# Performance work log

Measured on AMD Instinct MI355X. Metric: run time of the kernel, lower is better.

The kernel has to match this reference:

```python
import jax, jax.numpy as jnp
import numpy as np

SEQ_LEN = 2048
N_FFT = 4096  # nearest power of two >= 2*SEQ_LEN - 1
K = 24
D_IN = 512
D_OUT = 512
K_U = 3


def setup_inputs() -> dict:
    key = jax.random.key(0)
    k1, k2, k3, k4, k5 = jax.random.split(key, 5)
    x = jax.random.normal(k1, (1, SEQ_LEN, D_IN), dtype=jnp.float32)
    phi = jax.random.normal(k2, (SEQ_LEN, K), dtype=jnp.float32)
    M = jax.random.normal(k3, (D_OUT, D_IN, K_U), dtype=jnp.float32) / D_IN
    M_phi_plus = jax.random.normal(k4, (K, D_IN, D_OUT), dtype=jnp.float32) / 10.0
    M_phi_minus = jax.random.normal(k5, (K, D_IN, D_OUT), dtype=jnp.float32) / 10.0
    return {"x": x, "phi": phi, "M": M, "M_phi_plus": M_phi_plus, "M_phi_minus": M_phi_minus}


def _convolve(u, v, n):
    # u: (bsz, seq, d_in); v: (seq, K) spectral filters
    bsz, seq_len, d_in = u.shape
    Kf = v.shape[1]
    # alternating sign (+1, -1, +1, ...) along time, shape (1, seq, 1, 1)
    sgn = jnp.where(jnp.arange(seq_len) % 2 == 1, -1.0, 1.0).reshape(1, seq_len, 1, 1)
    v_f = jnp.fft.rfft(v.astype(jnp.float32).reshape(1, seq_len, Kf, 1, 1), n=n, axis=1)
    u_exp = jnp.broadcast_to(u[:, :, None, :], (bsz, seq_len, Kf, d_in))
    # stack [u, u*sgn] -> (bsz, seq, K, d_in, 2)
    U = jnp.stack([u_exp, u_exp * sgn], axis=-1).astype(jnp.float32)
    U_f = jnp.fft.rfft(U, n=n, axis=1)
    U_conv = jnp.fft.irfft(v_f * U_f, n=n, axis=1)[:, :seq_len]
    U_plus = U_conv[..., 0]
    U_minus = U_conv[..., 1] * sgn  # (b, seq, K, d_in) * (1, seq, 1, 1)
    return U_plus, U_minus


def _ar_preds(M, x):
    # M: (d_out, d_in, k_u); x: (b, l, d_in)
    # ar[t] = sum_{i=0}^{k_u-1} M[:,:,i] @ x[t-i]  (zero before start)
    b, l, _ = x.shape
    out = jnp.zeros((b, l, M.shape[0]), dtype=x.dtype)
    for i in range(M.shape[-1]):
        x_shift = jnp.pad(x, ((0, 0), (i, 0), (0, 0)))[:, :l]
        out = out + jnp.einsum("bli,oi->blo", x_shift, M[:, :, i])
    return out


def reference(x, phi, M, M_phi_plus, M_phi_minus):
    U_plus, U_minus = _convolve(x, phi, N_FFT)
    spectral_plus = jnp.einsum("blkd,kdo->blo", U_plus, M_phi_plus)
    spectral_minus = jnp.einsum("blkd,kdo->blo", U_minus, M_phi_minus)
    output = spectral_plus + spectral_minus  # use_hankel_L=False
    ar = _ar_preds(M, x)
    return output + ar
```

## Files before the change

kernel.cpp:

```cpp
#include <hip/hip_runtime.h>

typedef __bf16 bf16;
typedef bf16 bf16x8 __attribute__((ext_vector_type(8)));
typedef float floatx16 __attribute__((ext_vector_type(16)));

#define AS1 __attribute__((address_space(1)))
#define AS3 __attribute__((address_space(3)))

#define KTOT 26112

__device__ __forceinline__ void stage_tile(const bf16* g, int ld, bf16* lds, int tid) {
#pragma unroll
    for (int it = 0; it < 4; ++it) {
        int q    = it * 256 + tid;
        int row  = q >> 3;
        int col8 = (q & 7) ^ (row & 7);
        __builtin_amdgcn_global_load_lds(
            (const AS1 void*)(g + (size_t)row * ld + col8 * 8),
            (AS3 void*)(lds + q * 8), 16, 0, 0);
    }
}

__device__ __forceinline__ void mfma_block(const bf16* lA, const bf16* lB,
                                           floatx16 acc[2][2], int lane, int wm, int wn) {
    const int lrow = lane & 31;
    const int lk   = lane >> 5;
#pragma unroll
    for (int s = 0; s < 4; ++s) {
        bf16x8 af[2], bfr[2];
        const int c8 = s * 2 + lk;
#pragma unroll
        for (int mi = 0; mi < 2; ++mi) {
            int r = wm * 64 + mi * 32 + lrow;
            af[mi] = *(const bf16x8*)(lA + r * 64 + ((c8 ^ (r & 7)) << 3));
        }
#pragma unroll
        for (int ni = 0; ni < 2; ++ni) {
            int r = wn * 64 + ni * 32 + lrow;
            bfr[ni] = *(const bf16x8*)(lB + r * 64 + ((c8 ^ (r & 7)) << 3));
        }
#pragma unroll
        for (int mi = 0; mi < 2; ++mi)
#pragma unroll
            for (int ni = 0; ni < 2; ++ni)
                acc[mi][ni] = __builtin_amdgcn_mfma_f32_32x32x16_bf16(
                    af[mi], bfr[ni], acc[mi][ni], 0, 0, 0);
    }
}

#define CD_ROW(r, lane) (((r) & 3) + 8 * ((r) >> 2) + 4 * ((lane) >> 5))

__global__ __launch_bounds__(256) void conv_gemm(const bf16* __restrict__ Tb,
                                                 const bf16* __restrict__ xT2,
                                                 bf16* __restrict__ A2) {
    __shared__ bf16 lA[128 * 64], lB[128 * 64];
    const int tid = threadIdx.x;
    const int lane = tid & 63, wave = tid >> 6, wm = wave & 1, wn = wave >> 1;
    const int bid = blockIdx.x;
    const int a    = 7 - (bid / 384);
    const int rem  = bid % 384;
    const int dblk = rem / 48;
    const int kw   = rem % 48;

    floatx16 acc[2][2];
#pragma unroll
    for (int mi = 0; mi < 2; ++mi)
#pragma unroll
        for (int ni = 0; ni < 2; ++ni)
#pragma unroll
            for (int e = 0; e < 16; ++e) acc[mi][ni][e] = 0.f;

    for (int c = 0; c <= a; ++c) {
        const bf16* Ab = Tb + ((size_t)kw * 8 + (a - c)) * 16384;
        const bf16* Bb = xT2 + (size_t)(dblk * 128) * 1024 + c * 128;
#pragma unroll
        for (int kk = 0; kk < 128; kk += 64) {
            stage_tile(Ab + kk, 128, lA, tid);
            stage_tile(Bb + kk, 1024, lB, tid);
            __syncthreads();
            mfma_block(lA, lB, acc, lane, wm, wn);
            __syncthreads();
        }
    }
    const int w = kw & 1, k = kw >> 1;
    const int kv = w ? (24 + k) : k;
    const int p = dblk >> 2, dbase = (dblk & 3) * 128;
    bf16* Ocol = A2 + (size_t)kv * 512 + dbase;
#pragma unroll
    for (int mi = 0; mi < 2; ++mi)
#pragma unroll
        for (int ni = 0; ni < 2; ++ni)
#pragma unroll
            for (int r = 0; r < 16; ++r) {
                int tau = a * 128 + wm * 64 + mi * 32 + CD_ROW(r, lane);
                int t = 2 * tau + p + w;
                if (t < 2048) {
                    int col = wn * 64 + ni * 32 + (lane & 31);
                    Ocol[(size_t)t * KTOT + col] = (bf16)acc[mi][ni][r];
                }
            }
}

__global__ __launch_bounds__(256) void proj_gemm(const bf16* __restrict__ A2,
                                                 const bf16* __restrict__ B2,
                                                 float* __restrict__ P2) {
    __shared__ bf16 lA[128 * 64], lB[128 * 64];
    const int tid = threadIdx.x;
    const int lane = tid & 63, wave = tid >> 6, wm = wave & 1, wn = wave >> 1;
    const int bm = blockIdx.x, sp = blockIdx.y, bn = blockIdx.z;
    const bf16* Ab = A2 + (size_t)bm * 128 * KTOT + sp * 2176;
    const bf16* Bb = B2 + (size_t)bn * 128 * KTOT + sp * 2176;

    floatx16 acc[2][2];
#pragma unroll
    for (int mi = 0; mi < 2; ++mi)
#pragma unroll
        for (int ni = 0; ni < 2; ++ni)
#pragma unroll
            for (int e = 0; e < 16; ++e) acc[mi][ni][e] = 0.f;

    for (int kk = 0; kk < 2176; kk += 64) {
        stage_tile(Ab + kk, KTOT, lA, tid);
        stage_tile(Bb + kk, KTOT, lB, tid);
        __syncthreads();
        mfma_block(lA, lB, acc, lane, wm, wn);
        __syncthreads();
    }
    float* Pt = P2 + (size_t)sp * 1048576;
#pragma unroll
    for (int mi = 0; mi < 2; ++mi)
#pragma unroll
        for (int ni = 0; ni < 2; ++ni)
#pragma unroll
            for (int r = 0; r < 16; ++r) {
                int t = bm * 128 + wm * 64 + mi * 32 + CD_ROW(r, lane);
                int o = bn * 128 + wn * 64 + ni * 32 + (lane & 31);
                Pt[(size_t)t * 512 + o] = acc[mi][ni][r];
            }
}

__global__ void prep_all(const float* __restrict__ x, const float* __restrict__ phi,
                         const float* __restrict__ M, const float* __restrict__ Mp,
                         const float* __restrict__ Mm, bf16* __restrict__ xT2,
                         bf16* __restrict__ A2, bf16* __restrict__ B2,
                         bf16* __restrict__ Tb) {
    __shared__ float smem[64 * 65];
    const int b = blockIdx.x, tid = threadIdx.x;
    if (b < 256) {
        int dpt = (b >> 4) * 64, st = (b & 15) * 64;
        int p = dpt >> 9, dbase = dpt & 511;
#pragma unroll
        for (int it = 0; it < 16; ++it) {
            int q = it * 256 + tid;
            int r = q >> 6, cc = q & 63;
            smem[r * 65 + cc] = x[(size_t)(2 * (st + r) + p) * 512 + dbase + cc];
        }
        __syncthreads();
#pragma unroll
        for (int it = 0; it < 16; ++it) {
            int q = it * 256 + tid;
            int r = q >> 6, cc = q & 63;
            xT2[(size_t)(dpt + r) * 1024 + st + cc] = (bf16)smem[cc * 65 + r];
        }
    } else if (b < 1792) {
        int idx8 = (b - 256) * 256 + tid;
        int t = idx8 / 192, q = idx8 % 192;
        int i = q >> 6, d8 = (q & 63) * 8;
        bf16x8 v;
        if (t - i >= 0) {
            const float* xp = x + (size_t)(t - i) * 512 + d8;
#pragma unroll
            for (int jj = 0; jj < 8; ++jj) v[jj] = (bf16)xp[jj];
        } else {
#pragma unroll
            for (int jj = 0; jj < 8; ++jj) v[jj] = (bf16)0.f;
        }
        *(bf16x8*)(A2 + (size_t)t * KTOT + 24576 + i * 512 + d8) = v;
    } else if (b < 3328) {
        int b2 = b - 1792;
        int k = b2 >> 6, rem2 = b2 & 63;
        int dt = (rem2 >> 3) * 64, ot = (rem2 & 7) * 64;
        const float* Sp = Mp + (size_t)k * 262144;
        const float* Sm = Mm + (size_t)k * 262144;
#pragma unroll
        for (int it = 0; it < 16; ++it) {
            int q = it * 256 + tid;
            int r = q >> 6, cc = q & 63;
            smem[r * 65 + cc] = Sp[(size_t)(dt + r) * 512 + ot + cc];
        }
        __syncthreads();
        float m1[16];
#pragma unroll
        for (int it = 0; it < 16; ++it) {
            int q = it * 256 + tid;
            int r = q >> 6, cc = q & 63;
            m1[it] = smem[cc * 65 + r];
        }
        __syncthreads();
#pragma unroll
        for (int it = 0; it < 16; ++it) {
            int q = it * 256 + tid;
            int r = q >> 6, cc = q & 63;
            smem[r * 65 + cc] = Sm[(size_t)(dt + r) * 512 + ot + cc];
        }
        __syncthreads();
#pragma unroll
        for (int it = 0; it < 16; ++it) {
            int q = it * 256 + tid;
            int r = q >> 6, cc = q & 63;
            float m2 = smem[cc * 65 + r];
            B2[(size_t)(ot + r) * KTOT + k * 512 + dt + cc]        = (bf16)(m1[it] + m2);
            B2[(size_t)(ot + r) * KTOT + (24 + k) * 512 + dt + cc] = (bf16)(m1[it] - m2);
        }
    } else if (b < 3840) {
        int o = b - 3328;
        for (int q = tid; q < 1536; q += 256) smem[q] = M[(size_t)o * 1536 + q];
        __syncthreads();
        for (int q = tid; q < 1536; q += 256) {
            int i = q >> 9, d = q & 511;
            B2[(size_t)o * KTOT + 24576 + q] = (bf16)smem[d * 3 + i];
        }
    } else if (b < 4224) {
        int b3 = b - 3840;
        int kw = b3 >> 3, m = b3 & 7;
        int k = kw >> 1, w = kw & 1;
        if (tid < 255) {
            int sh = m * 128 - 127 + tid;
            smem[tid] = (sh >= 0) ? phi[(size_t)(2 * sh + w) * 24 + k] : 0.f;
        }
        __syncthreads();
        bf16* Tp = Tb + (size_t)b3 * 16384;
#pragma unroll
        for (int it = 0; it < 8; ++it) {
            int q = it * 256 + tid;
            int i = q >> 4, j8 = (q & 15) * 8;
            bf16x8 v;
#pragma unroll
            for (int jj = 0; jj < 8; ++jj)
                v[jj] = (bf16)smem[127 + i - (j8 + jj)];
            *(bf16x8*)(Tp + i * 128 + j8) = v;
        }
    } else {
        int off = 12288 + (b - 4224) * 2048 + tid * 8;
        bf16x8 z;
#pragma unroll
        for (int jj = 0; jj < 8; ++jj) z[jj] = (bf16)0.f;
        *(bf16x8*)(A2 + off) = z;
    }
}

__global__ void reduce12(const float* __restrict__ P2, float* __restrict__ out) {
    int idx = blockIdx.x * 256 + threadIdx.x;
    if (idx >= 2048 * 512) return;
    float s = 0.f;
#pragma unroll
    for (int sp = 0; sp < 12; ++sp)
        s += P2[(size_t)sp * 1048576 + idx];
    out[idx] = s;
}

extern "C" void kernel_launch(void* const* d_in, const int* in_sizes, int n_in,
                              void* d_out, int out_size, void* d_ws, size_t ws_size,
                              hipStream_t stream) {
    const float* x   = (const float*)d_in[0];
    const float* phi = (const float*)d_in[1];
    const float* M   = (const float*)d_in[2];
    const float* Mp  = (const float*)d_in[3];
    const float* Mm  = (const float*)d_in[4];
    float* out = (float*)d_out;
    char* ws = (char*)d_ws;

    bf16*  Tb  = (bf16*)(ws + 0);
    bf16*  xT2 = (bf16*)(ws + 12582912);
    bf16*  A2  = (bf16*)(ws + 14680064);
    bf16*  B2  = (bf16*)(ws + 121634816);
    float* P2  = (float*)(ws + 148373504);

    prep_all<<<4230, 256, 0, stream>>>(x, phi, M, Mp, Mm, xT2, A2, B2, Tb);
    conv_gemm<<<3072, 256, 0, stream>>>(Tb, xT2, A2);
    proj_gemm<<<dim3(16, 12, 4), 256, 0, stream>>>(A2, B2, P2);
    reduce12<<<4096, 256, 0, stream>>>(P2, out);
}
```

Before: 269.1 us.

## Double-buffer proj_gemm LDS, reduce split-K to 8, vectorize prep stores

proj_gemm now double-buffers its LDS tiles, so loads for the next K slice are issued while MFMAs run on the current one. The split-K factor drops from 12 to 8, giving larger K chunks, fewer partial buffers and a cheaper reduction, at the cost of fewer blocks (512 instead of 768). prep_all also gets vectorized bf16x8 stores for its transposes, float4 loads, and a single-pass load of both M_phi matrices into two shared buffers. The extra LDS per block (64KB for proj_gemm) may lower occupancy.

```diff
diff --git a/kernel.cpp b/kernel.cpp
--- a/kernel.cpp
+++ b/kernel.cpp
@@ -104,12 +104,12 @@
 __global__ __launch_bounds__(256) void proj_gemm(const bf16* __restrict__ A2,
                                                  const bf16* __restrict__ B2,
                                                  float* __restrict__ P2) {
-    __shared__ bf16 lA[128 * 64], lB[128 * 64];
+    __shared__ bf16 lA[2][128 * 64], lB[2][128 * 64];
     const int tid = threadIdx.x;
     const int lane = tid & 63, wave = tid >> 6, wm = wave & 1, wn = wave >> 1;
     const int bm = blockIdx.x, sp = blockIdx.y, bn = blockIdx.z;
-    const bf16* Ab = A2 + (size_t)bm * 128 * KTOT + sp * 2176;
-    const bf16* Bb = B2 + (size_t)bn * 128 * KTOT + sp * 2176;
+    const bf16* Ab = A2 + (size_t)bm * 128 * KTOT + sp * 3264;
+    const bf16* Bb = B2 + (size_t)bn * 128 * KTOT + sp * 3264;
 
     floatx16 acc[2][2];
 #pragma unroll
@@ -119,12 +119,18 @@
 #pragma unroll
             for (int e = 0; e < 16; ++e) acc[mi][ni][e] = 0.f;
 
-    for (int kk = 0; kk < 2176; kk += 64) {
-        stage_tile(Ab + kk, KTOT, lA, tid);
-        stage_tile(Bb + kk, KTOT, lB, tid);
-        __syncthreads();
-        mfma_block(lA, lB, acc, lane, wm, wn);
-        __syncthreads();
+    stage_tile(Ab, KTOT, lA[0], tid);
+    stage_tile(Bb, KTOT, lB[0], tid);
+    __syncthreads();
+    int cur = 0;
+    for (int kk = 0; kk < 3264; kk += 64) {
+        if (kk + 64 < 3264) {
+            stage_tile(Ab + kk + 64, KTOT, lA[cur ^ 1], tid);
+            stage_tile(Bb + kk + 64, KTOT, lB[cur ^ 1], tid);
+        }
+        mfma_block(lA[cur], lB[cur], acc, lane, wm, wn);
+        __syncthreads();
+        cur ^= 1;
     }
     float* Pt = P2 + (size_t)sp * 1048576;
 #pragma unroll
@@ -144,7 +150,7 @@
                          const float* __restrict__ Mm, bf16* __restrict__ xT2,
                          bf16* __restrict__ A2, bf16* __restrict__ B2,
                          bf16* __restrict__ Tb) {
-    __shared__ float smem[64 * 65];
+    __shared__ float smem[2][64 * 65];
     const int b = blockIdx.x, tid = threadIdx.x;
     if (b < 256) {
         int dpt = (b >> 4) * 64, st = (b & 15) * 64;
@@ -153,14 +159,18 @@
         for (int it = 0; it < 16; ++it) {
             int q = it * 256 + tid;
             int r = q >> 6, cc = q & 63;
-            smem[r * 65 + cc] = x[(size_t)(2 * (st + r) + p) * 512 + dbase + cc];
-        }
-        __syncthreads();
-#pragma unroll
-        for (int it = 0; it < 16; ++it) {
-            int q = it * 256 + tid;
-            int r = q >> 6, cc = q & 63;
-            xT2[(size_t)(dpt + r) * 1024 + st + cc] = (bf16)smem[cc * 65 + r];
+            smem[0][r * 65 + cc] = x[(size_t)(2 * (st + r) + p) * 512 + dbase + cc];
+        }
+        __syncthreads();
+#pragma unroll
+        for (int it = 0; it < 2; ++it) {
+            int q = it * 256 + tid;
+            int r = q >> 3, c8 = q & 7;
+            bf16x8 v;
+#pragma unroll
+            for (int jj = 0; jj < 8; ++jj)
+                v[jj] = (bf16)smem[0][(c8 * 8 + jj) * 65 + r];
+            *(bf16x8*)&xT2[(size_t)(dpt + r) * 1024 + st + c8 * 8] = v;
         }
     } else if (b < 1792) {
         int idx8 = (b - 256) * 256 + tid;
@@ -169,8 +179,10 @@
         bf16x8 v;
         if (t - i >= 0) {
             const float* xp = x + (size_t)(t - i) * 512 + d8;
-#pragma unroll
-            for (int jj = 0; jj < 8; ++jj) v[jj] = (bf16)xp[jj];
+            float4 f0 = *(const float4*)(xp);
+            float4 f1 = *(const float4*)(xp + 4);
+            v[0] = (bf16)f0.x; v[1] = (bf16)f0.y; v[2] = (bf16)f0.z; v[3] = (bf16)f0.w;
+            v[4] = (bf16)f1.x; v[5] = (bf16)f1.y; v[6] = (bf16)f1.z; v[7] = (bf16)f1.w;
         } else {
 #pragma unroll
             for (int jj = 0; jj < 8; ++jj) v[jj] = (bf16)0.f;
@@ -186,39 +198,36 @@
         for (int it = 0; it < 16; ++it) {
             int q = it * 256 + tid;
             int r = q >> 6, cc = q & 63;
-            smem[r * 65 + cc] = Sp[(size_t)(dt + r) * 512 + ot + cc];
-        }
-        __syncthreads();
-        float m1[16];
-#pragma unroll
-        for (int it = 0; it < 16; ++it) {
-            int q = it * 256 + tid;
-            int r = q >> 6, cc = q & 63;
-            m1[it] = smem[cc * 65 + r];
-        }
-        __syncthreads();
-#pragma unroll
-        for (int it = 0; it < 16; ++it) {
-            int q = it * 256 + tid;
-            int r = q >> 6, cc = q & 63;
-            smem[r * 65 + cc] = Sm[(size_t)(dt + r) * 512 + ot + cc];
-        }
-        __syncthreads();
-#pragma unroll
-        for (int it = 0; it < 16; ++it) {
-            int q = it * 256 + tid;
-            int r = q >> 6, cc = q & 63;
-            float m2 = smem[cc * 65 + r];
-            B2[(size_t)(ot + r) * KTOT + k * 512 + dt + cc]        = (bf16)(m1[it] + m2);
-            B2[(size_t)(ot + r) * KTOT + (24 + k) * 512 + dt + cc] = (bf16)(m1[it] - m2);
+            smem[0][r * 65 + cc] = Sp[(size_t)(dt + r) * 512 + ot + cc];
+            smem[1][r * 65 + cc] = Sm[(size_t)(dt + r) * 512 + ot + cc];
+        }
+        __syncthreads();
+#pragma unroll
+        for (int it = 0; it < 2; ++it) {
+            int q = it * 256 + tid;
+            int r = q >> 3, c8 = q & 7;
+            bf16x8 vs, vd;
+#pragma unroll
+            for (int jj = 0; jj < 8; ++jj) {
+                float av = smem[0][(c8 * 8 + jj) * 65 + r];
+                float bv = smem[1][(c8 * 8 + jj) * 65 + r];
+                vs[jj] = (bf16)(av + bv);
+                vd[jj] = (bf16)(av - bv);
+            }
+            *(bf16x8*)&B2[(size_t)(ot + r) * KTOT + k * 512 + dt + c8 * 8] = vs;
+            *(bf16x8*)&B2[(size_t)(ot + r) * KTOT + (24 + k) * 512 + dt + c8 * 8] = vd;
         }
     } else if (b < 3840) {
         int o = b - 3328;
-        for (int q = tid; q < 1536; q += 256) smem[q] = M[(size_t)o * 1536 + q];
-        __syncthreads();
-        for (int q = tid; q < 1536; q += 256) {
-            int i = q >> 9, d = q & 511;
-            B2[(size_t)o * KTOT + 24576 + q] = (bf16)smem[d * 3 + i];
+        for (int q = tid; q < 1536; q += 256) smem[0][q] = M[(size_t)o * 1536 + q];
+        __syncthreads();
+        if (tid < 192) {
+            int q = tid * 8;
+            int i = q >> 9, d0 = q & 511;
+            bf16x8 v;
+#pragma unroll
+            for (int jj = 0; jj < 8; ++jj) v[jj] = (bf16)smem[0][(d0 + jj) * 3 + i];
+            *(bf16x8*)&B2[(size_t)o * KTOT + 24576 + q] = v;
         }
     } else if (b < 4224) {
         int b3 = b - 3840;
@@ -226,7 +235,7 @@
         int k = kw >> 1, w = kw & 1;
         if (tid < 255) {
             int sh = m * 128 - 127 + tid;
-            smem[tid] = (sh >= 0) ? phi[(size_t)(2 * sh + w) * 24 + k] : 0.f;
+            smem[0][tid] = (sh >= 0) ? phi[(size_t)(2 * sh + w) * 24 + k] : 0.f;
         }
         __syncthreads();
         bf16* Tp = Tb + (size_t)b3 * 16384;
@@ -237,7 +246,7 @@
             bf16x8 v;
 #pragma unroll
             for (int jj = 0; jj < 8; ++jj)
-                v[jj] = (bf16)smem[127 + i - (j8 + jj)];
+                v[jj] = (bf16)smem[0][127 + i - (j8 + jj)];
             *(bf16x8*)(Tp + i * 128 + j8) = v;
         }
     } else {
@@ -249,12 +258,12 @@
     }
 }
 
-__global__ void reduce12(const float* __restrict__ P2, float* __restrict__ out) {
+__global__ void reduce8(const float* __restrict__ P2, float* __restrict__ out) {
     int idx = blockIdx.x * 256 + threadIdx.x;
     if (idx >= 2048 * 512) return;
     float s = 0.f;
 #pragma unroll
-    for (int sp = 0; sp < 12; ++sp)
+    for (int sp = 0; sp < 8; ++sp)
         s += P2[(size_t)sp * 1048576 + idx];
     out[idx] = s;
 }
@@ -278,6 +287,6 @@
 
     prep_all<<<4230, 256, 0, stream>>>(x, phi, M, Mp, Mm, xT2, A2, B2, Tb);
     conv_gemm<<<3072, 256, 0, stream>>>(Tb, xT2, A2);
-    proj_gemm<<<dim3(16, 12, 4), 256, 0, stream>>>(A2, B2, P2);
-    reduce12<<<4096, 256, 0, stream>>>(P2, out);
-}
+    proj_gemm<<<dim3(16, 8, 4), 256, 0, stream>>>(A2, B2, P2);
+    reduce8<<<4096, 256, 0, stream>>>(P2, out);
+}
```

New measurement: 252.9 us. 6.0% less time.
